# Performance work log

Measured on AMD Instinct MI355X. Metric: run time of the kernel, lower is better.

## Reference

```python
import jax, jax.numpy as jnp
import numpy as np

DIM = 1024
HEADS = 16
WINDOW = 5
B, S = 2, 2048
EPS = 1e-5


def setup_inputs() -> dict:
    key = jax.random.key(0)
    ks = jax.random.split(key, 12)
    d = DIM
    sc = lambda n: 1.0 / np.sqrt(n)
    return {
        "x": jax.random.normal(ks[0], (B, S, d), dtype=jnp.float32),
        "w_in": jax.random.normal(ks[1], (3 * d, d), dtype=jnp.float32) * sc(d),
        "b_in": jnp.zeros((3 * d,), dtype=jnp.float32),
        "w_out": jax.random.normal(ks[2], (d, d), dtype=jnp.float32) * sc(d),
        "b_out": jnp.zeros((d,), dtype=jnp.float32),
        "ln1_g": jnp.ones((d,), dtype=jnp.float32),
        "ln1_b": jnp.zeros((d,), dtype=jnp.float32),
        "ln2_g": jnp.ones((d,), dtype=jnp.float32),
        "ln2_b": jnp.zeros((d,), dtype=jnp.float32),
        "w1": jax.random.normal(ks[3], (4 * d, d), dtype=jnp.float32) * sc(d),
        "b1": jnp.zeros((4 * d,), dtype=jnp.float32),
        "w2": jax.random.normal(ks[4], (d, 4 * d), dtype=jnp.float32) * sc(4 * d),
        "b2": jnp.zeros((d,), dtype=jnp.float32),
    }


def _layernorm(x, g, b):
    mu = jnp.mean(x, axis=-1, keepdims=True)
    var = jnp.mean((x - mu) ** 2, axis=-1, keepdims=True)
    return (x - mu) * jax.lax.rsqrt(var + EPS) * g + b


def reference(x, w_in, b_in, w_out, b_out, ln1_g, ln1_b, ln2_g, ln2_b, w1, b1, w2, b2):
    Bq, Sq, d = x.shape
    hd = d // HEADS
    # in-projection (torch MHA: qkv = x @ W_in^T + b_in)
    qkv = jnp.einsum('bsd,ed->bse', x, w_in) + b_in  # [B,S,3d]
    q, k, v = jnp.split(qkv, 3, axis=-1)
    q = q.reshape(Bq, Sq, HEADS, hd)
    k = k.reshape(Bq, Sq, HEADS, hd)
    v = v.reshape(Bq, Sq, HEADS, hd)
    scale = 1.0 / np.sqrt(hd)
    scores = jnp.einsum('bqhd,bkhd->bhqk', q, k) * scale  # [B,H,S,S]
    # local causal mask: row i attends to j in [i-window+1, i]
    i = jnp.arange(Sq)[:, None]
    j = jnp.arange(Sq)[None, :]
    allowed = (j <= i) & (j > i - WINDOW)
    scores = jnp.where(allowed, scores, jnp.float32(-jnp.inf))
    probs = jax.nn.softmax(scores, axis=-1)
    attn = jnp.einsum('bhqk,bkhd->bqhd', probs, v).reshape(Bq, Sq, d)
    attn = jnp.einsum('bsd,ed->bse', attn, w_out) + b_out
    x1 = _layernorm(x + attn, ln1_g, ln1_b)
    h = jax.nn.gelu(jnp.einsum('bsd,ed->bse', x1, w1) + b1, approximate=False)
    mlp = jnp.einsum('bse,de->bsd', h, w2) + b2
    return _layernorm(x1 + mlp, ln2_g, ln2_b)
```

## Files before the change

kernel.cpp:

```cpp
#include <hip/hip_runtime.h>
#include <hip/hip_bf16.h>
#include <math.h>

typedef __hip_bfloat16 bf16;
typedef __attribute__((ext_vector_type(8))) short bf16x8;
typedef __attribute__((ext_vector_type(4))) float f32x4;

#define GPTR(p) ((const __attribute__((address_space(1))) void*)(p))
#define LPTR(p) ((__attribute__((address_space(3))) void*)(p))

__device__ __forceinline__ float b2f(short s) {
  unsigned int u = ((unsigned int)(unsigned short)s) << 16;
  float f; __builtin_memcpy(&f, &u, 4); return f;
}

__global__ __launch_bounds__(256) void cvt_all(
    const float* __restrict__ x,    const float* __restrict__ w_in,
    const float* __restrict__ w_out,const float* __restrict__ w1,
    const float* __restrict__ w2,
    bf16* __restrict__ xb,   bf16* __restrict__ winb, bf16* __restrict__ woutb,
    bf16* __restrict__ w1b,  bf16* __restrict__ w2b)
{
  const int b = blockIdx.x;
  const float* in; bf16* out; int base;
  if      (b <  4096) { in = x;     out = xb;    base = 0; }
  else if (b <  7168) { in = w_in;  out = winb;  base = 4096; }
  else if (b <  8192) { in = w_out; out = woutb; base = 7168; }
  else if (b < 12288) { in = w1;    out = w1b;   base = 8192; }
  else                { in = w2;    out = w2b;   base = 12288; }
  const int i = ((b - base) * 256 + threadIdx.x) * 4;
  const float4 f = *(const float4*)(in + i);
  ushort4 u;
  u.x = __bfloat16_as_ushort(__float2bfloat16(f.x));
  u.y = __bfloat16_as_ushort(__float2bfloat16(f.y));
  u.z = __bfloat16_as_ushort(__float2bfloat16(f.z));
  u.w = __bfloat16_as_ushort(__float2bfloat16(f.w));
  *(ushort4*)(out + i) = u;
}

__device__ __forceinline__ float gelu_fast(float v) {
  const float u  = 1.5957691216f * (v + 0.044715f * v * v * v);
  const float e  = __expf(u);
  return v * e / (e + 1.0f);
}

template<int GELU, int RESID>
__global__ __launch_bounds__(256, 4) void gemm_bt(
    const bf16* __restrict__ A, int lda,
    const bf16* __restrict__ B, int ldb,
    const float* __restrict__ bias,
    const void* __restrict__ Rv, int ldr,
    bf16* __restrict__ C, int ldc, long czstride,
    int M, int N, int kchunk)
{
  __shared__ __align__(16) bf16 As[128 * 64];
  __shared__ __align__(16) bf16 Bs[128 * 64];

  const int t    = threadIdx.x;
  const int lane = t & 63;
  const int w    = t >> 6;
  const int wm   = w >> 1;
  const int wn   = w & 1;
  const int lr   = lane & 15;
  const int lq   = lane >> 4;
  const int m0   = blockIdx.y * 128;
  const int n0   = blockIdx.x * 128;
  const int kz   = blockIdx.z;

  A += (size_t)kz * kchunk;
  B += (size_t)kz * kchunk;
  C += (size_t)kz * czstride;

  f32x4 acc[4][4];
  #pragma unroll
  for (int mi = 0; mi < 4; ++mi)
    #pragma unroll
    for (int ni = 0; ni < 4; ++ni)
      acc[mi][ni] = (f32x4){0.f, 0.f, 0.f, 0.f};

  const int wbase = (t & ~63) * 8;

  for (int k0 = 0; k0 < kchunk; k0 += 64) {
    #pragma unroll
    for (int it = 0; it < 4; ++it) {
      const int c    = it * 256 + t;
      const int row  = c >> 3;
      const int csw  = ((c & 7) ^ (row & 7)) << 3;
      const bf16* ga = A + (size_t)(m0 + row) * lda + k0 + csw;
      const bf16* gb = B + (size_t)(n0 + row) * ldb + k0 + csw;
      __builtin_amdgcn_global_load_lds(GPTR(ga), LPTR(&As[it * 2048 + wbase]), 16, 0, 0);
      __builtin_amdgcn_global_load_lds(GPTR(gb), LPTR(&Bs[it * 2048 + wbase]), 16, 0, 0);
    }
    __syncthreads();

    #pragma unroll
    for (int ks = 0; ks < 2; ++ks) {
      const int swz = (((ks * 4 + lq) ^ (lr & 7)) << 3);
      bf16x8 af[4], bfr[4];
      #pragma unroll
      for (int mi = 0; mi < 4; ++mi)
        af[mi] = *(const bf16x8*)&As[(wm * 64 + mi * 16 + lr) * 64 + swz];
      #pragma unroll
      for (int ni = 0; ni < 4; ++ni)
        bfr[ni] = *(const bf16x8*)&Bs[(wn * 64 + ni * 16 + lr) * 64 + swz];
      #pragma unroll
      for (int mi = 0; mi < 4; ++mi)
        #pragma unroll
        for (int ni = 0; ni < 4; ++ni)
          acc[mi][ni] = __builtin_amdgcn_mfma_f32_16x16x32_bf16(af[mi], bfr[ni], acc[mi][ni], 0, 0, 0);
    }
    __syncthreads();
  }

  #pragma unroll
  for (int ni = 0; ni < 4; ++ni) {
    const int col = n0 + wn * 64 + ni * 16 + lr;
    const float bv = bias ? bias[col] : 0.f;
    #pragma unroll
    for (int mi = 0; mi < 4; ++mi) {
      const int rowb = m0 + wm * 64 + mi * 16 + lq * 4;
      #pragma unroll
      for (int i = 0; i < 4; ++i) {
        float v = acc[mi][ni][i] + bv;
        if (GELU) v = gelu_fast(v);
        if (RESID == 1) v += ((const float*)Rv)[(size_t)(rowb + i) * ldr + col];
        if (RESID == 2) v += __bfloat162float(((const bf16*)Rv)[(size_t)(rowb + i) * ldr + col]);
        C[(size_t)(rowb + i) * ldc + col] = __float2bfloat16(v);
      }
    }
  }
}

__global__ __launch_bounds__(256) void attn_win(bf16* __restrict__ qkv)
{
  const int lane = threadIdx.x & 63;
  const int tk   = blockIdx.x * 4 + (threadIdx.x >> 6);
  const int s    = tk & 2047;
  const int doff = (lane >> 2) * 64 + (lane & 3) * 16;

  const size_t row = (size_t)tk * 3072;

  bf16x8 qa = *(const bf16x8*)&qkv[row + doff];
  bf16x8 qb = *(const bf16x8*)&qkv[row + doff + 8];
  float qf[16];
  #pragma unroll
  for (int e = 0; e < 8; ++e) { qf[e] = b2f(qa[e]); qf[8 + e] = b2f(qb[e]); }

  const int W = (s + 1 < 5) ? (s + 1) : 5;
  float p[5];
  #pragma unroll
  for (int j = 0; j < 5; ++j) {
    const int jc = (j < W) ? j : 0;
    const size_t kr = row - (size_t)jc * 3072 + 1024;
    bf16x8 ka = *(const bf16x8*)&qkv[kr + doff];
    bf16x8 kb = *(const bf16x8*)&qkv[kr + doff + 8];
    float d = 0.f;
    #pragma unroll
    for (int e = 0; e < 8; ++e) d += qf[e] * b2f(ka[e]);
    #pragma unroll
    for (int e = 0; e < 8; ++e) d += qf[8 + e] * b2f(kb[e]);
    d += __shfl_xor(d, 1);
    d += __shfl_xor(d, 2);
    p[j] = (j < W) ? d * 0.125f : -1e30f;
  }

  float mx = fmaxf(fmaxf(fmaxf(p[0], p[1]), fmaxf(p[2], p[3])), p[4]);
  float sum = 0.f;
  #pragma unroll
  for (int j = 0; j < 5; ++j) { p[j] = __expf(p[j] - mx); sum += p[j]; }
  const float inv = 1.f / sum;

  float o[16];
  #pragma unroll
  for (int e = 0; e < 16; ++e) o[e] = 0.f;
  #pragma unroll
  for (int j = 0; j < 5; ++j) {
    const int jc = (j < W) ? j : 0;
    const size_t vr = row - (size_t)jc * 3072 + 2048;
    bf16x8 va = *(const bf16x8*)&qkv[vr + doff];
    bf16x8 vb = *(const bf16x8*)&qkv[vr + doff + 8];
    #pragma unroll
    for (int e = 0; e < 8; ++e) { o[e] += p[j] * b2f(va[e]); o[8 + e] += p[j] * b2f(vb[e]); }
  }

  bf16x8 oa, ob;
  #pragma unroll
  for (int e = 0; e < 8; ++e) {
    oa[e] = (short)__bfloat16_as_ushort(__float2bfloat16(o[e] * inv));
    ob[e] = (short)__bfloat16_as_ushort(__float2bfloat16(o[8 + e] * inv));
  }
  *(bf16x8*)&qkv[row + doff]     = oa;
  *(bf16x8*)&qkv[row + doff + 8] = ob;
}

template<int OUTF32, int RESBF16>
__global__ __launch_bounds__(256) void ln_fuse(
    const bf16* __restrict__ P0, const bf16* __restrict__ P1, int ldp,
    const void* __restrict__ Rv,
    const float* __restrict__ bias,
    const float* __restrict__ g, const float* __restrict__ bt,
    void* __restrict__ outv)
{
  const int tk   = blockIdx.x * 4 + (threadIdx.x >> 6);
  const int lane = threadIdx.x & 63;
  const size_t bp = (size_t)tk * ldp;
  const size_t bo = (size_t)tk * 1024;

  float v[16];
  float sum = 0.f;
  #pragma unroll
  for (int i = 0; i < 16; ++i) {
    const int e = i * 64 + lane;
    float t = __bfloat162float(P0[bp + e]) + __bfloat162float(P1[bp + e]) + bias[e];
    if (RESBF16) t += __bfloat162float(((const bf16*)Rv)[bo + e]);
    else         t += ((const float*)Rv)[bo + e];
    v[i] = t;
    sum += t;
  }
  #pragma unroll
  for (int d = 1; d < 64; d <<= 1) sum += __shfl_xor(sum, d);
  const float mu = sum * (1.f / 1024.f);

  float sq = 0.f;
  #pragma unroll
  for (int i = 0; i < 16; ++i) { const float dv = v[i] - mu; sq += dv * dv; }
  #pragma unroll
  for (int d = 1; d < 64; d <<= 1) sq += __shfl_xor(sq, d);
  const float rstd = rsqrtf(sq * (1.f / 1024.f) + 1e-5f);

  #pragma unroll
  for (int i = 0; i < 16; ++i) {
    const int e = i * 64 + lane;
    const float o = (v[i] - mu) * rstd * g[e] + bt[e];
    if (OUTF32) ((float*)outv)[bo + e] = o;
    else        ((bf16*)outv)[bo + e] = __float2bfloat16(o);
  }
}

extern "C" void kernel_launch(void* const* d_in, const int* in_sizes, int n_in,
                              void* d_out, int out_size, void* d_ws, size_t ws_size,
                              hipStream_t stream)
{
  const float* x     = (const float*)d_in[0];
  const float* w_in  = (const float*)d_in[1];
  const float* b_in  = (const float*)d_in[2];
  const float* w_out = (const float*)d_in[3];
  const float* b_out = (const float*)d_in[4];
  const float* ln1_g = (const float*)d_in[5];
  const float* ln1_b = (const float*)d_in[6];
  const float* ln2_g = (const float*)d_in[7];
  const float* ln2_b = (const float*)d_in[8];
  const float* w1    = (const float*)d_in[9];
  const float* b1    = (const float*)d_in[10];
  const float* w2    = (const float*)d_in[11];
  const float* b2    = (const float*)d_in[12];
  float* out = (float*)d_out;

  char* ws = (char*)d_ws;
  bf16* qkv     = (bf16*)(ws);
  bf16* h       = (bf16*)(ws);
  bf16* x_b     = (bf16*)(ws + 33554432);
  bf16* x1_b    = (bf16*)(ws + 41943040);
  bf16* w1_b    = (bf16*)(ws + 50331648);
  bf16* w2_b    = (bf16*)(ws + 58720256);
  bf16* w_in_b  = (bf16*)(ws + 67108864);
  bf16* w_out_b = (bf16*)(ws + 73400320);
  bf16* P0      = x_b;
  bf16* P1      = w1_b;

  const dim3 blk(256);

  cvt_all<<<dim3(16384), blk, 0, stream>>>(x, w_in, w_out, w1, w2,
                                           x_b, w_in_b, w_out_b, w1_b, w2_b);

  gemm_bt<0,0><<<dim3(24, 32, 1), blk, 0, stream>>>(
      x_b, 1024, w_in_b, 1024, b_in, nullptr, 0, qkv, 3072, 0, 4096, 3072, 1024);
  attn_win<<<dim3(1024), blk, 0, stream>>>(qkv);
  gemm_bt<0,0><<<dim3(8, 32, 2), blk, 0, stream>>>(
      qkv, 3072, w_out_b, 1024, nullptr, nullptr, 0,
      qkv + 1024, 3072, 1024, 4096, 1024, 512);
  ln_fuse<0,0><<<dim3(1024), blk, 0, stream>>>(
      qkv + 1024, qkv + 2048, 3072, x, b_out, ln1_g, ln1_b, x1_b);
  gemm_bt<1,0><<<dim3(32, 32, 1), blk, 0, stream>>>(
      x1_b, 1024, w1_b, 1024, b1, nullptr, 0, h, 4096, 0, 4096, 4096, 1024);
  gemm_bt<0,0><<<dim3(8, 32, 2), blk, 0, stream>>>(
      h, 4096, w2_b, 4096, nullptr, nullptr, 0,
      P0, 1024, 8388608, 4096, 1024, 2048);
  ln_fuse<1,1><<<dim3(1024), blk, 0, stream>>>(
      P0, P1, 1024, x1_b, b2, ln2_g, ln2_b, out);
}
```

Baseline: 285.6 us.

## Rewrite GEMM as 8-wave 128x256 tile with triple-buffered LDS pipeline

Replaces the 256-thread 128x128 GEMM with a 512-thread kernel that computes 128x256 tiles. It triple-buffers LDS so global-to-LDS loads run two k-steps ahead, and splits each k-step into two phases that interleave loads with MFMA work under barriers and s_setprio. It also remaps workgroup IDs so neighbouring tiles land on the same XCD, for better L2 locality. The aim is to hide memory latency and raise MFMA utilisation. The cost is 144KB of LDS, which limits occupancy, and the hand-tuned waitcnt logic is fragile.

```diff
diff --git a/kernel.cpp b/kernel.cpp
--- a/kernel.cpp
+++ b/kernel.cpp
@@ -44,33 +44,89 @@
   return v * e / (e + 1.0f);
 }
 
+#define STAGE(bi, kt, j)                                                      \
+  do {                                                                        \
+    if ((j) < 4)                                                              \
+      __builtin_amdgcn_global_load_lds(                                       \
+          GPTR(B + (size_t)gsrcB[(j)] + ((kt) << 6)),                         \
+          LPTR(&lds[(bi)][8192 + (j) * 4096 + ldsW]), 16, 0, 0);              \
+    else                                                                      \
+      __builtin_amdgcn_global_load_lds(                                       \
+          GPTR(A + (size_t)gsrcA[(j) - 4] + ((kt) << 6)),                     \
+          LPTR(&lds[(bi)][((j) - 4) * 4096 + ldsW]), 16, 0, 0);               \
+  } while (0)
+
+#define LDSRD(off) (*(const bf16x8*)((const char*)(&lds[bi][0]) + (off)))
+
 template<int GELU, int RESID>
-__global__ __launch_bounds__(256, 4) void gemm_bt(
+__global__ __launch_bounds__(512, 2) void gemm8p(
     const bf16* __restrict__ A, int lda,
     const bf16* __restrict__ B, int ldb,
     const float* __restrict__ bias,
     const void* __restrict__ Rv, int ldr,
     bf16* __restrict__ C, int ldc, long czstride,
-    int M, int N, int kchunk)
-{
-  __shared__ __align__(16) bf16 As[128 * 64];
-  __shared__ __align__(16) bf16 Bs[128 * 64];
+    int kchunk)
+{
+  __shared__ __align__(16) bf16 lds[3][24576];
 
   const int t    = threadIdx.x;
   const int lane = t & 63;
   const int w    = t >> 6;
-  const int wm   = w >> 1;
-  const int wn   = w & 1;
+  const int wm   = w >> 2;
+  const int wn   = w & 3;
   const int lr   = lane & 15;
   const int lq   = lane >> 4;
-  const int m0   = blockIdx.y * 128;
-  const int n0   = blockIdx.x * 128;
-  const int kz   = blockIdx.z;
+
+  const int gx   = gridDim.x, gy = gridDim.y;
+  const int nwg  = gx * gy * gridDim.z;
+  const int orig = blockIdx.x + gx * (blockIdx.y + gy * blockIdx.z);
+  const int qq   = nwg >> 3, rr = nwg & 7;
+  const int xcd  = orig & 7;
+  const int wid  = (xcd < rr ? xcd * (qq + 1) : rr * (qq + 1) + (xcd - rr) * qq)
+                 + (orig >> 3);
+  const int n0 = (wid % gx) * 256;
+  const int m0 = ((wid / gx) % gy) * 128;
+  const int kz = wid / (gx * gy);
 
   A += (size_t)kz * kchunk;
   B += (size_t)kz * kchunk;
   C += (size_t)kz * czstride;
 
+  const int NT = kchunk >> 6;
+
+  int gsrcA[2], gsrcB[4];
+  #pragma unroll
+  for (int j = 0; j < 4; ++j) {
+    const int q   = j * 8192 + t * 16;
+    const int row = q >> 7;
+    const int qs  = q ^ ((row & 7) << 4);
+    gsrcB[j] = (n0 + (qs >> 7)) * ldb + ((qs & 127) >> 1);
+  }
+  #pragma unroll
+  for (int j = 0; j < 2; ++j) {
+    const int q   = j * 8192 + t * 16;
+    const int row = q >> 7;
+    const int qs  = q ^ ((row & 7) << 4);
+    gsrcA[j] = (m0 + (qs >> 7)) * lda + ((qs & 127) >> 1);
+  }
+  const int ldsW = w * 512;
+
+  int aoff[4][2], boff[4][2];
+  #pragma unroll
+  for (int mi = 0; mi < 4; ++mi) {
+    const int row = wm * 64 + mi * 16 + lr;
+    #pragma unroll
+    for (int ks = 0; ks < 2; ++ks)
+      aoff[mi][ks] = (row * 128 + ks * 64 + lq * 16) ^ ((row & 7) << 4);
+  }
+  #pragma unroll
+  for (int ni = 0; ni < 4; ++ni) {
+    const int row = wn * 64 + ni * 16 + lr;
+    #pragma unroll
+    for (int ks = 0; ks < 2; ++ks)
+      boff[ni][ks] = 16384 + ((row * 128 + ks * 64 + lq * 16) ^ ((row & 7) << 4));
+  }
+
   f32x4 acc[4][4];
   #pragma unroll
   for (int mi = 0; mi < 4; ++mi)
@@ -78,38 +134,72 @@
     for (int ni = 0; ni < 4; ++ni)
       acc[mi][ni] = (f32x4){0.f, 0.f, 0.f, 0.f};
 
-  const int wbase = (t & ~63) * 8;
-
-  for (int k0 = 0; k0 < kchunk; k0 += 64) {
-    #pragma unroll
-    for (int it = 0; it < 4; ++it) {
-      const int c    = it * 256 + t;
-      const int row  = c >> 3;
-      const int csw  = ((c & 7) ^ (row & 7)) << 3;
-      const bf16* ga = A + (size_t)(m0 + row) * lda + k0 + csw;
-      const bf16* gb = B + (size_t)(n0 + row) * ldb + k0 + csw;
-      __builtin_amdgcn_global_load_lds(GPTR(ga), LPTR(&As[it * 2048 + wbase]), 16, 0, 0);
-      __builtin_amdgcn_global_load_lds(GPTR(gb), LPTR(&Bs[it * 2048 + wbase]), 16, 0, 0);
+  STAGE(0, 0, 0); STAGE(0, 0, 1); STAGE(0, 0, 2);
+  STAGE(0, 0, 3); STAGE(0, 0, 4); STAGE(0, 0, 5);
+  if (NT > 1) {
+    STAGE(1, 1, 0); STAGE(1, 1, 1); STAGE(1, 1, 2);
+    STAGE(1, 1, 3); STAGE(1, 1, 4); STAGE(1, 1, 5);
+    asm volatile("s_waitcnt vmcnt(6)" ::: "memory");
+  } else {
+    asm volatile("s_waitcnt vmcnt(0)" ::: "memory");
+  }
+  __builtin_amdgcn_s_barrier();
+
+  for (int kt = 0; kt < NT; ++kt) {
+    const int  bi = kt % 3;
+    const int  si = (kt + 2) % 3;
+    const bool st = (kt + 2) < NT;
+
+    bf16x8 af[2][2], bq[4][2];
+
+    #pragma unroll
+    for (int mi = 0; mi < 2; ++mi) {
+      af[mi][0] = LDSRD(aoff[mi][0]);
+      af[mi][1] = LDSRD(aoff[mi][1]);
     }
-    __syncthreads();
-
-    #pragma unroll
-    for (int ks = 0; ks < 2; ++ks) {
-      const int swz = (((ks * 4 + lq) ^ (lr & 7)) << 3);
-      bf16x8 af[4], bfr[4];
-      #pragma unroll
-      for (int mi = 0; mi < 4; ++mi)
-        af[mi] = *(const bf16x8*)&As[(wm * 64 + mi * 16 + lr) * 64 + swz];
+    #pragma unroll
+    for (int ni = 0; ni < 4; ++ni) {
+      bq[ni][0] = LDSRD(boff[ni][0]);
+      bq[ni][1] = LDSRD(boff[ni][1]);
+    }
+    if (st) { STAGE(si, kt + 2, 0); STAGE(si, kt + 2, 1); STAGE(si, kt + 2, 2); }
+    __builtin_amdgcn_s_barrier();
+    asm volatile("s_waitcnt lgkmcnt(0)" ::: "memory");
+    __builtin_amdgcn_sched_barrier(0);
+    __builtin_amdgcn_s_setprio(1);
+    #pragma unroll
+    for (int mi = 0; mi < 2; ++mi)
       #pragma unroll
       for (int ni = 0; ni < 4; ++ni)
-        bfr[ni] = *(const bf16x8*)&Bs[(wn * 64 + ni * 16 + lr) * 64 + swz];
+        #pragma unroll
+        for (int ks = 0; ks < 2; ++ks)
+          acc[mi][ni] = __builtin_amdgcn_mfma_f32_16x16x32_bf16(
+              af[mi][ks], bq[ni][ks], acc[mi][ni], 0, 0, 0);
+    __builtin_amdgcn_s_setprio(0);
+    __builtin_amdgcn_s_barrier();
+
+    #pragma unroll
+    for (int mi = 0; mi < 2; ++mi) {
+      af[mi][0] = LDSRD(aoff[2 + mi][0]);
+      af[mi][1] = LDSRD(aoff[2 + mi][1]);
+    }
+    if (st) { STAGE(si, kt + 2, 3); STAGE(si, kt + 2, 4); STAGE(si, kt + 2, 5); }
+    __builtin_amdgcn_s_barrier();
+    asm volatile("s_waitcnt lgkmcnt(0)" ::: "memory");
+    __builtin_amdgcn_sched_barrier(0);
+    __builtin_amdgcn_s_setprio(1);
+    #pragma unroll
+    for (int mi = 0; mi < 2; ++mi)
       #pragma unroll
-      for (int mi = 0; mi < 4; ++mi)
+      for (int ni = 0; ni < 4; ++ni)
         #pragma unroll
-        for (int ni = 0; ni < 4; ++ni)
-          acc[mi][ni] = __builtin_amdgcn_mfma_f32_16x16x32_bf16(af[mi], bfr[ni], acc[mi][ni], 0, 0, 0);
-    }
-    __syncthreads();
+        for (int ks = 0; ks < 2; ++ks)
+          acc[2 + mi][ni] = __builtin_amdgcn_mfma_f32_16x16x32_bf16(
+              af[mi][ks], bq[ni][ks], acc[2 + mi][ni], 0, 0, 0);
+    __builtin_amdgcn_s_setprio(0);
+    if (kt < NT - 2)       asm volatile("s_waitcnt vmcnt(6)" ::: "memory");
+    else if (kt == NT - 2) asm volatile("s_waitcnt vmcnt(0)" ::: "memory");
+    __builtin_amdgcn_s_barrier();
   }
 
   #pragma unroll
@@ -269,23 +359,24 @@
   bf16* P1      = w1_b;
 
   const dim3 blk(256);
+  const dim3 blk512(512);
 
   cvt_all<<<dim3(16384), blk, 0, stream>>>(x, w_in, w_out, w1, w2,
                                            x_b, w_in_b, w_out_b, w1_b, w2_b);
 
-  gemm_bt<0,0><<<dim3(24, 32, 1), blk, 0, stream>>>(
-      x_b, 1024, w_in_b, 1024, b_in, nullptr, 0, qkv, 3072, 0, 4096, 3072, 1024);
+  gemm8p<0,0><<<dim3(12, 32, 1), blk512, 0, stream>>>(
+      x_b, 1024, w_in_b, 1024, b_in, nullptr, 0, qkv, 3072, 0, 1024);
   attn_win<<<dim3(1024), blk, 0, stream>>>(qkv);
-  gemm_bt<0,0><<<dim3(8, 32, 2), blk, 0, stream>>>(
+  gemm8p<0,0><<<dim3(4, 32, 2), blk512, 0, stream>>>(
       qkv, 3072, w_out_b, 1024, nullptr, nullptr, 0,
-      qkv + 1024, 3072, 1024, 4096, 1024, 512);
+      qkv + 1024, 3072, 1024, 512);
   ln_fuse<0,0><<<dim3(1024), blk, 0, stream>>>(
       qkv + 1024, qkv + 2048, 3072, x, b_out, ln1_g, ln1_b, x1_b);
-  gemm_bt<1,0><<<dim3(32, 32, 1), blk, 0, stream>>>(
-      x1_b, 1024, w1_b, 1024, b1, nullptr, 0, h, 4096, 0, 4096, 4096, 1024);
-  gemm_bt<0,0><<<dim3(8, 32, 2), blk, 0, stream>>>(
+  gemm8p<1,0><<<dim3(16, 32, 1), blk512, 0, stream>>>(
+      x1_b, 1024, w1_b, 1024, b1, nullptr, 0, h, 4096, 0, 1024);
+  gemm8p<0,0><<<dim3(4, 32, 2), blk512, 0, stream>>>(
       h, 4096, w2_b, 4096, nullptr, nullptr, 0,
-      P0, 1024, 8388608, 4096, 1024, 2048);
+      P0, 1024, 8388608, 2048);
   ln_fuse<1,1><<<dim3(1024), blk, 0, stream>>>(
       P0, P1, 1024, x1_b, b2, ln2_g, ln2_b, out);
 }
```

Result: slower. 302.9 us (+6.1%).

## Add 256x256 pipelined MFMA GEMM with direct-to-LDS loads for large projections

Applied to the files above, without the earlier changes.

Adds a 512-thread GEMM kernel with 256x256 output tiles, double-buffered LDS filled by global_load_lds, XOR-swizzled layout, an XCD-aware workgroup remap and interleaved barriers/setprio around MFMA groups. The QKV, FFN1 and FFN2 projections now use it, with FFN2 split four ways along K. The first LayerNorm writes an fp32 copy of x1 into the output buffer so the final LayerNorm can sum four partials plus an fp32 residual. Larger tiles raise data reuse and cut global traffic, but they also produce fewer workgroups (192 for QKV), which risks poor CU occupancy, and the split-K partials add write and read traffic.

```diff
diff --git a/kernel.cpp b/kernel.cpp
--- a/kernel.cpp
+++ b/kernel.cpp
@@ -43,6 +43,177 @@
   const float e  = __expf(u);
   return v * e / (e + 1.0f);
 }
+
+#define RD(BUF, OFF) (*(const bf16x8*)(((const char*)lds) + (BUF)*65536 + (OFF)))
+#define STG(GP, SRC, LOFF)                                                    \
+  __builtin_amdgcn_global_load_lds(GPTR((GP) + (SRC)),                        \
+                                   LPTR(((char*)lds) + (LOFF)), 16, 0, 0)
+#define STGH(BUF, REGBASE, GP, SARR, KT) do {                                 \
+    STG(GP, SARR[0] + ((KT) << 6), (BUF)*65536 + (REGBASE) + ldst);           \
+    STG(GP, SARR[1] + ((KT) << 6), (BUF)*65536 + (REGBASE) + 8192 + ldst);    \
+  } while (0)
+#define MFMA8(MB, NB, AF, BF)                                                 \
+    _Pragma("unroll") for (int mi = 0; mi < 4; ++mi)                          \
+      _Pragma("unroll") for (int ni = 0; ni < 2; ++ni)                        \
+        _Pragma("unroll") for (int ks = 0; ks < 2; ++ks)                      \
+          acc[(MB)+mi][(NB)+ni] = __builtin_amdgcn_mfma_f32_16x16x32_bf16(    \
+              AF[mi][ks], BF[ni][ks], acc[(MB)+mi][(NB)+ni], 0, 0, 0);
+
+#define KTILE(T, BUF) do {                                                    \
+    bf16x8 af[4][2], bl[2][2], bh[2][2];                                      \
+    _Pragma("unroll") for (int mi = 0; mi < 4; ++mi) {                        \
+      af[mi][0] = RD(BUF, aoff[mi][0]); af[mi][1] = RD(BUF, aoff[mi][1]); }   \
+    _Pragma("unroll") for (int ni = 0; ni < 2; ++ni) {                        \
+      bl[ni][0] = RD(BUF, boff[ni][0]); bl[ni][1] = RD(BUF, boff[ni][1]); }   \
+    if ((T) + 1 < NT) STGH((BUF)^1, 49152, B, bHiS, (T)+1);                   \
+    asm volatile("s_waitcnt lgkmcnt(8)" ::: "memory");                        \
+    __builtin_amdgcn_s_barrier();                                             \
+    asm volatile("s_waitcnt lgkmcnt(0)" ::: "memory");                        \
+    __builtin_amdgcn_sched_barrier(0);                                        \
+    __builtin_amdgcn_s_setprio(1);                                            \
+    MFMA8(0, 0, af, bl);                                                      \
+    __builtin_amdgcn_s_setprio(0);                                            \
+    __builtin_amdgcn_s_barrier();                                             \
+    _Pragma("unroll") for (int ni = 0; ni < 2; ++ni) {                        \
+      bh[ni][0] = RD(BUF, boff[2+ni][0]); bh[ni][1] = RD(BUF, boff[2+ni][1]); }\
+    if ((T) + 1 < NT) STGH((BUF)^1, 16384, A, aHiS, (T)+1);                   \
+    __builtin_amdgcn_s_barrier();                                             \
+    asm volatile("s_waitcnt lgkmcnt(0)" ::: "memory");                        \
+    __builtin_amdgcn_sched_barrier(0);                                        \
+    __builtin_amdgcn_s_setprio(1);                                            \
+    MFMA8(0, 2, af, bh);                                                      \
+    __builtin_amdgcn_s_setprio(0);                                            \
+    __builtin_amdgcn_s_barrier();                                             \
+    _Pragma("unroll") for (int mi = 0; mi < 4; ++mi) {                        \
+      af[mi][0] = RD(BUF, aoff[4+mi][0]); af[mi][1] = RD(BUF, aoff[4+mi][1]); }\
+    if ((T) + 2 < NT) STGH(BUF, 32768, B, bLoS, (T)+2);                       \
+    __builtin_amdgcn_s_barrier();                                             \
+    asm volatile("s_waitcnt lgkmcnt(0)" ::: "memory");                        \
+    __builtin_amdgcn_sched_barrier(0);                                        \
+    __builtin_amdgcn_s_setprio(1);                                            \
+    MFMA8(4, 0, af, bl);                                                      \
+    __builtin_amdgcn_s_setprio(0);                                            \
+    __builtin_amdgcn_s_barrier();                                             \
+    if ((T) + 2 < NT) STGH(BUF, 0, A, aLoS, (T)+2);                           \
+    __builtin_amdgcn_s_setprio(1);                                            \
+    MFMA8(4, 2, af, bh);                                                      \
+    __builtin_amdgcn_s_setprio(0);                                            \
+    if ((T) < NT - 2)       asm volatile("s_waitcnt vmcnt(4)" ::: "memory");  \
+    else if ((T) == NT - 2) asm volatile("s_waitcnt vmcnt(0)" ::: "memory");  \
+    __builtin_amdgcn_s_barrier();                                             \
+  } while (0)
+
+template<int GELU>
+__global__ __launch_bounds__(512, 2) void gemm256(
+    const bf16* __restrict__ A, int lda,
+    const bf16* __restrict__ B, int ldb,
+    const float* __restrict__ bias,
+    bf16* __restrict__ C, int ldc, long czstride, bf16* __restrict__ Clast,
+    int kchunk)
+{
+  __shared__ __align__(16) bf16 lds[2][32768];
+
+  const int t    = threadIdx.x;
+  const int lane = t & 63;
+  const int w    = t >> 6;
+  const int wm   = w >> 2;
+  const int wn   = w & 3;
+  const int lr   = lane & 15;
+  const int lq   = lane >> 4;
+
+  const int gx   = gridDim.x, gy = gridDim.y, gz = gridDim.z;
+  const int nwg  = gx * gy * gz;
+  const int orig = blockIdx.x + gx * (blockIdx.y + gy * blockIdx.z);
+  const int qq   = nwg >> 3, rr = nwg & 7;
+  const int xcd  = orig & 7;
+  const int wid  = (xcd < rr ? xcd * (qq + 1) : rr * (qq + 1) + (xcd - rr) * qq)
+                 + (orig >> 3);
+  const int n0 = (wid % gx) * 256;
+  const int m0 = ((wid / gx) % gy) * 256;
+  const int kz = wid / (gx * gy);
+
+  A += (size_t)kz * kchunk;
+  B += (size_t)kz * kchunk;
+  if (Clast && kz == gz - 1) C = Clast; else C += (size_t)kz * czstride;
+
+  const int NT = kchunk >> 6;
+
+  int aLoS[2], aHiS[2], bLoS[2], bHiS[2];
+  #pragma unroll
+  for (int r = 0; r < 2; ++r) {
+    const int q   = r * 8192 + t * 16;
+    const int row = q >> 7;
+    const int col = ((q & 127) ^ ((row & 7) << 4)) >> 1;
+    aLoS[r] = (m0 + row) * lda + col;
+    aHiS[r] = (m0 + 128 + row) * lda + col;
+    bLoS[r] = (n0 + row) * ldb + col;
+    bHiS[r] = (n0 + 128 + row) * ldb + col;
+  }
+  const int ldst = t * 16;
+
+  int aoff[8][2], boff[4][2];
+  #pragma unroll
+  for (int mi = 0; mi < 8; ++mi) {
+    const int row = wm * 128 + mi * 16 + lr;
+    #pragma unroll
+    for (int ks = 0; ks < 2; ++ks)
+      aoff[mi][ks] = row * 128 + ((ks * 64 + lq * 16) ^ ((row & 7) << 4));
+  }
+  #pragma unroll
+  for (int ni = 0; ni < 4; ++ni) {
+    const int row = wn * 64 + ni * 16 + lr;
+    #pragma unroll
+    for (int ks = 0; ks < 2; ++ks)
+      boff[ni][ks] = 32768 + row * 128 + ((ks * 64 + lq * 16) ^ ((row & 7) << 4));
+  }
+
+  f32x4 acc[8][4];
+  #pragma unroll
+  for (int mi = 0; mi < 8; ++mi)
+    #pragma unroll
+    for (int ni = 0; ni < 4; ++ni)
+      acc[mi][ni] = (f32x4){0.f, 0.f, 0.f, 0.f};
+
+  STGH(0, 32768, B, bLoS, 0);
+  STGH(0, 0,     A, aLoS, 0);
+  STGH(0, 49152, B, bHiS, 0);
+  STGH(0, 16384, A, aHiS, 0);
+  if (NT > 1) {
+    STGH(1, 32768, B, bLoS, 1);
+    STGH(1, 0,     A, aLoS, 1);
+    asm volatile("s_waitcnt vmcnt(4)" ::: "memory");
+  } else {
+    asm volatile("s_waitcnt vmcnt(0)" ::: "memory");
+  }
+  __builtin_amdgcn_s_barrier();
+
+  for (int T = 0; T < NT; T += 2) {
+    KTILE(T, 0);
+    KTILE(T + 1, 1);
+  }
+
+  #pragma unroll
+  for (int ni = 0; ni < 4; ++ni) {
+    const int col = n0 + wn * 64 + ni * 16 + lr;
+    const float bv = bias ? bias[col] : 0.f;
+    #pragma unroll
+    for (int mi = 0; mi < 8; ++mi) {
+      const int rowb = m0 + wm * 128 + mi * 16 + lq * 4;
+      #pragma unroll
+      for (int i = 0; i < 4; ++i) {
+        float v = acc[mi][ni][i] + bv;
+        if (GELU) v = gelu_fast(v);
+        C[(size_t)(rowb + i) * ldc + col] = __float2bfloat16(v);
+      }
+    }
+  }
+}
+
+#undef KTILE
+#undef MFMA8
+#undef STGH
+#undef STG
+#undef RD
 
 template<int GELU, int RESID>
 __global__ __launch_bounds__(256, 4) void gemm_bt(
@@ -193,13 +364,13 @@
   *(bf16x8*)&qkv[row + doff + 8] = ob;
 }
 
-template<int OUTF32, int RESBF16>
-__global__ __launch_bounds__(256) void ln_fuse(
+template<int DUAL>
+__global__ __launch_bounds__(256) void ln_fuse2(
     const bf16* __restrict__ P0, const bf16* __restrict__ P1, int ldp,
-    const void* __restrict__ Rv,
+    const float* __restrict__ Rv,
     const float* __restrict__ bias,
     const float* __restrict__ g, const float* __restrict__ bt,
-    void* __restrict__ outv)
+    bf16* __restrict__ out_bf, float* __restrict__ out_f32)
 {
   const int tk   = blockIdx.x * 4 + (threadIdx.x >> 6);
   const int lane = threadIdx.x & 63;
@@ -211,11 +382,10 @@
   #pragma unroll
   for (int i = 0; i < 16; ++i) {
     const int e = i * 64 + lane;
-    float t = __bfloat162float(P0[bp + e]) + __bfloat162float(P1[bp + e]) + bias[e];
-    if (RESBF16) t += __bfloat162float(((const bf16*)Rv)[bo + e]);
-    else         t += ((const float*)Rv)[bo + e];
-    v[i] = t;
-    sum += t;
+    float tv = __bfloat162float(P0[bp + e]) + __bfloat162float(P1[bp + e])
+             + bias[e] + Rv[bo + e];
+    v[i] = tv;
+    sum += tv;
   }
   #pragma unroll
   for (int d = 1; d < 64; d <<= 1) sum += __shfl_xor(sum, d);
@@ -232,8 +402,50 @@
   for (int i = 0; i < 16; ++i) {
     const int e = i * 64 + lane;
     const float o = (v[i] - mu) * rstd * g[e] + bt[e];
-    if (OUTF32) ((float*)outv)[bo + e] = o;
-    else        ((bf16*)outv)[bo + e] = __float2bfloat16(o);
+    out_bf[bo + e] = __float2bfloat16(o);
+    if (DUAL) out_f32[bo + e] = o;
+  }
+}
+
+__global__ __launch_bounds__(256) void ln_fuse4(
+    const bf16* __restrict__ Pb, long pstr, const bf16* __restrict__ P3,
+    const float* __restrict__ Rv,
+    const float* __restrict__ bias,
+    const float* __restrict__ g, const float* __restrict__ bt,
+    float* __restrict__ out)
+{
+  const int tk   = blockIdx.x * 4 + (threadIdx.x >> 6);
+  const int lane = threadIdx.x & 63;
+  const size_t bo = (size_t)tk * 1024;
+
+  float v[16];
+  float sum = 0.f;
+  #pragma unroll
+  for (int i = 0; i < 16; ++i) {
+    const size_t e = bo + i * 64 + lane;
+    const int eb = i * 64 + lane;
+    float tv = __bfloat162float(Pb[e]) + __bfloat162float(Pb[e + pstr])
+             + __bfloat162float(Pb[e + 2 * pstr]) + __bfloat162float(P3[e])
+             + bias[eb] + Rv[e];
+    v[i] = tv;
+    sum += tv;
+  }
+  #pragma unroll
+  for (int d = 1; d < 64; d <<= 1) sum += __shfl_xor(sum, d);
+  const float mu = sum * (1.f / 1024.f);
+
+  float sq = 0.f;
+  #pragma unroll
+  for (int i = 0; i < 16; ++i) { const float dv = v[i] - mu; sq += dv * dv; }
+  #pragma unroll
+  for (int d = 1; d < 64; d <<= 1) sq += __shfl_xor(sq, d);
+  const float rstd = rsqrtf(sq * (1.f / 1024.f) + 1e-5f);
+
+  #pragma unroll
+  for (int i = 0; i < 16; ++i) {
+    const size_t e = bo + i * 64 + lane;
+    const int eb = i * 64 + lane;
+    out[e] = (v[i] - mu) * rstd * g[eb] + bt[eb];
   }
 }
 
@@ -265,27 +477,27 @@
   bf16* w2_b    = (bf16*)(ws + 58720256);
   bf16* w_in_b  = (bf16*)(ws + 67108864);
   bf16* w_out_b = (bf16*)(ws + 73400320);
-  bf16* P0      = x_b;
-  bf16* P1      = w1_b;
+  bf16* Pbase   = x_b;
+  bf16* Plast   = w_in_b;
 
   const dim3 blk(256);
+  const dim3 blk512(512);
 
   cvt_all<<<dim3(16384), blk, 0, stream>>>(x, w_in, w_out, w1, w2,
                                            x_b, w_in_b, w_out_b, w1_b, w2_b);
 
-  gemm_bt<0,0><<<dim3(24, 32, 1), blk, 0, stream>>>(
-      x_b, 1024, w_in_b, 1024, b_in, nullptr, 0, qkv, 3072, 0, 4096, 3072, 1024);
+  gemm256<0><<<dim3(12, 16, 1), blk512, 0, stream>>>(
+      x_b, 1024, w_in_b, 1024, b_in, qkv, 3072, 0, nullptr, 1024);
   attn_win<<<dim3(1024), blk, 0, stream>>>(qkv);
   gemm_bt<0,0><<<dim3(8, 32, 2), blk, 0, stream>>>(
       qkv, 3072, w_out_b, 1024, nullptr, nullptr, 0,
       qkv + 1024, 3072, 1024, 4096, 1024, 512);
-  ln_fuse<0,0><<<dim3(1024), blk, 0, stream>>>(
-      qkv + 1024, qkv + 2048, 3072, x, b_out, ln1_g, ln1_b, x1_b);
-  gemm_bt<1,0><<<dim3(32, 32, 1), blk, 0, stream>>>(
-      x1_b, 1024, w1_b, 1024, b1, nullptr, 0, h, 4096, 0, 4096, 4096, 1024);
-  gemm_bt<0,0><<<dim3(8, 32, 2), blk, 0, stream>>>(
-      h, 4096, w2_b, 4096, nullptr, nullptr, 0,
-      P0, 1024, 8388608, 4096, 1024, 2048);
-  ln_fuse<1,1><<<dim3(1024), blk, 0, stream>>>(
-      P0, P1, 1024, x1_b, b2, ln2_g, ln2_b, out);
-}
+  ln_fuse2<1><<<dim3(1024), blk, 0, stream>>>(
+      qkv + 1024, qkv + 2048, 3072, x, b_out, ln1_g, ln1_b, x1_b, out);
+  gemm256<1><<<dim3(16, 16, 1), blk512, 0, stream>>>(
+      x1_b, 1024, w1_b, 1024, b1, h, 4096, 0, nullptr, 1024);
+  gemm256<0><<<dim3(4, 16, 4), blk512, 0, stream>>>(
+      h, 4096, w2_b, 4096, nullptr, Pbase, 1024, 4194304, Plast, 1024);
+  ln_fuse4<<<dim3(1024), blk, 0, stream>>>(
+      Pbase, 4194304, Plast, out, b2, ln2_g, ln2_b, out);
+}
```

After: 309.0 us. 8.2% more time.
